# Optimization experiments

Measured on AMD Instinct MI355X. Metric: run time of the kernel, lower is better.

## Reference

```python
import jax, jax.numpy as jnp
import numpy as np

D_MODEL = 1024
D_FF = 4096
NUM_EXPERTS = 8
TOP_K = 2


def setup_inputs() -> dict:
    key = jax.random.key(0)
    ks = jax.random.split(key, 9)
    s_in = 1.0 / np.sqrt(D_MODEL)
    s_ff = 1.0 / np.sqrt(D_FF)
    return {
        "x": jax.random.normal(ks[0], (2, 1024, D_MODEL), dtype=jnp.float32),
        "Wg": jax.random.uniform(ks[1], (D_MODEL, NUM_EXPERTS), minval=-s_in, maxval=s_in, dtype=jnp.float32),
        "bg": jax.random.uniform(ks[2], (NUM_EXPERTS,), minval=-s_in, maxval=s_in, dtype=jnp.float32),
        "W1": jax.random.uniform(ks[3], (NUM_EXPERTS, D_MODEL, D_FF), minval=-s_in, maxval=s_in, dtype=jnp.float32),
        "b1": jax.random.uniform(ks[4], (NUM_EXPERTS, D_FF), minval=-s_in, maxval=s_in, dtype=jnp.float32),
        "W2": jax.random.uniform(ks[5], (NUM_EXPERTS, D_MODEL, D_FF), minval=-s_in, maxval=s_in, dtype=jnp.float32),
        "b2": jax.random.uniform(ks[6], (NUM_EXPERTS, D_FF), minval=-s_in, maxval=s_in, dtype=jnp.float32),
        "W3": jax.random.uniform(ks[7], (NUM_EXPERTS, D_FF, D_MODEL), minval=-s_ff, maxval=s_ff, dtype=jnp.float32),
        "b3": jax.random.uniform(ks[8], (NUM_EXPERTS, D_MODEL), minval=-s_ff, maxval=s_ff, dtype=jnp.float32),
    }


def reference(x, Wg, bg, W1, b1, W2, b2, W3, b3):
    B, S, D = x.shape
    xf = x.reshape(-1, D)                                   # [N, D]
    N = xf.shape[0]

    # ---- Router (eval mode: no noise) ----
    logits = xf @ Wg + bg                                   # [N, E]
    top_logits, top_idx = jax.lax.top_k(logits, TOP_K)      # [N, K]
    top_w = jax.nn.softmax(top_logits, axis=-1)             # softmax over the top-k logits
    # scatter top-k weights into dense [N, E]; indices are unique per row
    comb_w = jnp.zeros_like(logits).at[jnp.arange(N)[:, None], top_idx].set(top_w)

    # ---- Experts: GLU-MLP, dense per-expert (weights are 0 for unrouted tokens) ----
    h1 = jnp.einsum('nd,edf->enf', xf, W1) + b1[:, None, :]  # [E, N, F]
    h2 = jnp.einsum('nd,edf->enf', xf, W2) + b2[:, None, :]
    hidden = jax.nn.gelu(h1, approximate=False) * h2         # torch nn.GELU is exact (erf)
    expert_out = jnp.einsum('enf,efd->end', hidden, W3) + b3[:, None, :]  # [E, N, D]

    # ---- Weighted combine ----
    final = jnp.einsum('end,ne->nd', expert_out, comb_w)     # [N, D]
    aux_loss = 0.0  # eval mode: aux loss inactive
    return final.reshape(B, S, D), aux_loss
```

## Files before the change

### kernel.cpp

```cpp
#include <hip/hip_runtime.h>
#include <hip/hip_bf16.h>
#include <math.h>

#define D_MODEL 1024
#define D_FF    4096
#define NE      8
#define MT      256

typedef __bf16 bf16x8 __attribute__((ext_vector_type(8)));
typedef float  f32x4  __attribute__((ext_vector_type(4)));

__device__ __forceinline__ void async16(const void* g, void* l) {
    __builtin_amdgcn_global_load_lds(
        (__attribute__((address_space(1))) uint32_t*)g,
        (__attribute__((address_space(3))) uint32_t*)l, 16, 0, 0);
}

__global__ __launch_bounds__(256) void router_kernel(
    const float* __restrict__ x, const float* __restrict__ Wg,
    const float* __restrict__ bg, int* __restrict__ topidx,
    float* __restrict__ topw, __bf16* __restrict__ Xb)
{
    int n = blockIdx.x, tid = threadIdx.x;
    const float* xr = x + (size_t)n * D_MODEL;
    int d0 = tid * 4;
    float4 xv = *reinterpret_cast<const float4*>(xr + d0);

    union { __bf16 h[4]; ushort4 u; } pk;
    pk.h[0] = (__bf16)xv.x; pk.h[1] = (__bf16)xv.y;
    pk.h[2] = (__bf16)xv.z; pk.h[3] = (__bf16)xv.w;
    *reinterpret_cast<ushort4*>(Xb + (size_t)n * D_MODEL + d0) = pk.u;

    float part[NE];
#pragma unroll
    for (int e = 0; e < NE; ++e) part[e] = 0.f;
    float xs[4] = {xv.x, xv.y, xv.z, xv.w};
#pragma unroll
    for (int j = 0; j < 4; ++j) {
        const float4* wr = reinterpret_cast<const float4*>(Wg + (size_t)(d0 + j) * NE);
        float4 w0 = wr[0], w1 = wr[1];
        part[0] += xs[j] * w0.x; part[1] += xs[j] * w0.y;
        part[2] += xs[j] * w0.z; part[3] += xs[j] * w0.w;
        part[4] += xs[j] * w1.x; part[5] += xs[j] * w1.y;
        part[6] += xs[j] * w1.z; part[7] += xs[j] * w1.w;
    }
#pragma unroll
    for (int off = 32; off > 0; off >>= 1) {
#pragma unroll
        for (int e = 0; e < NE; ++e) part[e] += __shfl_down(part[e], off);
    }
    __shared__ float sred[4][NE];
    __shared__ float slog[NE];
    int wave = tid >> 6, lane = tid & 63;
    if (lane == 0) {
#pragma unroll
        for (int e = 0; e < NE; ++e) sred[wave][e] = part[e];
    }
    __syncthreads();
    if (tid < NE)
        slog[tid] = bg[tid] + sred[0][tid] + sred[1][tid] + sred[2][tid] + sred[3][tid];
    __syncthreads();
    if (tid == 0) {
        float m0 = -1e30f, m1 = -1e30f; int i0 = 0, i1 = 0;
        for (int e = 0; e < NE; ++e) {
            float l = slog[e];
            if (l > m0)      { m1 = m0; i1 = i0; m0 = l; i0 = e; }
            else if (l > m1) { m1 = l;  i1 = e; }
        }
        float w1 = expf(m1 - m0);
        float s  = 1.f + w1;
        topidx[n * 2 + 0] = i0; topidx[n * 2 + 1] = i1;
        topw[n * 2 + 0] = 1.f / s; topw[n * 2 + 1] = w1 / s;
    }
}

__global__ __launch_bounds__(256) void build_lists_kernel(
    const int* __restrict__ topidx, const float* __restrict__ topw,
    int* __restrict__ pairTok, float* __restrict__ pairW,
    int* __restrict__ rbe, int* __restrict__ pairRow,
    int npairs, int maxrows, int maxblk)
{
    __shared__ int cnt[NE], cur[NE], pof[NE];
    int tid = threadIdx.x;
    if (tid < NE) { cnt[tid] = 0; cur[tid] = 0; }
    for (int i = tid; i < maxrows; i += 256) pairTok[i] = -1;
    for (int i = tid; i < maxblk; i += 256) rbe[i] = -1;
    __syncthreads();
    for (int p = tid; p < npairs; p += 256) atomicAdd(&cnt[topidx[p]], 1);
    __syncthreads();
    if (tid == 0) {
        int off = 0;
        for (int e = 0; e < NE; ++e) { pof[e] = off; off += (cnt[e] + MT - 1) & ~(MT - 1); }
        for (int e = 0; e < NE; ++e) {
            int nb = (cnt[e] + MT - 1) / MT;
            for (int j = 0; j < nb; ++j) rbe[pof[e] / MT + j] = e;
        }
    }
    __syncthreads();
    for (int p = tid; p < npairs; p += 256) {
        int e = topidx[p];
        int pos = atomicAdd(&cur[e], 1);
        int r = pof[e] + pos;
        pairTok[r]  = p >> 1;
        pairW[r]    = topw[p];
        pairRow[p]  = r;
    }
}

__global__ __launch_bounds__(256) void transpose_cvt_kernel(
    const float* __restrict__ src, __bf16* __restrict__ dst, int K, int N)
{
    const float* s = src + (size_t)blockIdx.z * K * N;
    __bf16*      d = dst + (size_t)blockIdx.z * K * N;
    int kt = blockIdx.y * 64, nt = blockIdx.x * 64;
    __shared__ float tile[64][65];
    int tid = threadIdx.x;
    int tr = tid >> 4, tc = (tid & 15) * 4;
#pragma unroll
    for (int it = 0; it < 4; ++it) {
        float4 v = *reinterpret_cast<const float4*>(
            s + (size_t)(kt + tr + it * 16) * N + nt + tc);
        tile[tr + it * 16][tc + 0] = v.x;
        tile[tr + it * 16][tc + 1] = v.y;
        tile[tr + it * 16][tc + 2] = v.z;
        tile[tr + it * 16][tc + 3] = v.w;
    }
    __syncthreads();
    int kq = (tid & 15) * 4;
#pragma unroll
    for (int it = 0; it < 4; ++it) {
        int rr = (tid >> 4) + it * 16;
        union { __bf16 h[4]; ushort4 u; } pk;
        pk.h[0] = (__bf16)tile[kq + 0][rr];
        pk.h[1] = (__bf16)tile[kq + 1][rr];
        pk.h[2] = (__bf16)tile[kq + 2][rr];
        pk.h[3] = (__bf16)tile[kq + 3][rr];
        *reinterpret_cast<ushort4*>(d + (size_t)(nt + rr) * K + kt + kq) = pk.u;
    }
}

__global__ __launch_bounds__(512, 4) void gemm1_mfma(
    const __bf16* __restrict__ Xb, const __bf16* __restrict__ W1t,
    const __bf16* __restrict__ W2t, const float* __restrict__ b1,
    const float* __restrict__ b2, const int* __restrict__ pairTok,
    const int* __restrict__ rbe, const __bf16* __restrict__ zpg,
    __bf16* __restrict__ hidden)
{
    int b = blockIdx.x;
    int e = rbe[b];
    if (e < 0) return;
    int fblk = blockIdx.y * 64;

    __shared__ __bf16 smem[2][12288];

    int tid = threadIdx.x, w = tid >> 6, l = tid & 63;
    int r0 = b * MT;
    int ss4 = (l & 3) ^ ((l >> 3) & 3);

    const __bf16* aptr[2];
#pragma unroll
    for (int j = 0; j < 2; ++j) {
        int row = w * 32 + j * 16 + (l >> 2);
        int tok = pairTok[r0 + row];
        aptr[j] = (tok >= 0 ? Xb + (size_t)tok * D_MODEL : zpg) + ss4 * 8;
    }
    const __bf16* wsrc = (w < 4) ? W1t : W2t;
    int wb = w & 3;
    const __bf16* bptr = wsrc + ((size_t)e << 22)
        + (size_t)(fblk + wb * 16 + (l >> 2)) * D_MODEL + ss4 * 8;
    int bdst = (w < 4 ? 8192 : 10240) + wb * 512;

    int wm = (w >> 1) * 64, wf = (w & 1) * 32;
    int lm = l & 15;
    int sl = (((l >> 4) ^ ((lm >> 1) & 3)) << 3);

    f32x4 c1[4][2], c2[4][2];
#pragma unroll
    for (int mi = 0; mi < 4; ++mi)
#pragma unroll
        for (int fj = 0; fj < 2; ++fj) {
            c1[mi][fj] = (f32x4){0.f, 0.f, 0.f, 0.f};
            c2[mi][fj] = (f32x4){0.f, 0.f, 0.f, 0.f};
        }

    auto stage = [&](int buf, int k0) {
        __bf16* base = &smem[buf][0];
        async16(aptr[0] + k0, base + w * 1024 + l * 8);
        async16(aptr[1] + k0, base + w * 1024 + 512 + l * 8);
        async16(bptr + k0, base + bdst + l * 8);
    };

    stage(0, 0);
    __syncthreads();
    const int NT = D_MODEL / 32;
    for (int t = 0; t < NT; ++t) {
        int cur = t & 1;
        if (t + 1 < NT) stage(cur ^ 1, (t + 1) * 32);
        const __bf16* sb = &smem[cur][0];
        bf16x8 a[4];
#pragma unroll
        for (int mi = 0; mi < 4; ++mi)
            a[mi] = *reinterpret_cast<const bf16x8*>(sb + (wm + mi * 16 + lm) * 32 + sl);
#pragma unroll
        for (int fj = 0; fj < 2; ++fj) {
            int frow = (wf + fj * 16 + lm) * 32 + sl;
            bf16x8 bv1 = *reinterpret_cast<const bf16x8*>(sb + 8192 + frow);
            bf16x8 bv2 = *reinterpret_cast<const bf16x8*>(sb + 10240 + frow);
#pragma unroll
            for (int mi = 0; mi < 4; ++mi) {
                c1[mi][fj] = __builtin_amdgcn_mfma_f32_16x16x32_bf16(a[mi], bv1, c1[mi][fj], 0, 0, 0);
                c2[mi][fj] = __builtin_amdgcn_mfma_f32_16x16x32_bf16(a[mi], bv2, c2[mi][fj], 0, 0, 0);
            }
        }
        __syncthreads();
    }

#pragma unroll
    for (int fj = 0; fj < 2; ++fj) {
        int f = fblk + wf + fj * 16 + lm;
        float b1v = b1[e * D_FF + f];
        float b2v = b2[e * D_FF + f];
#pragma unroll
        for (int mi = 0; mi < 4; ++mi)
#pragma unroll
            for (int r = 0; r < 4; ++r) {
                int m = wm + mi * 16 + (l >> 4) * 4 + r;
                float h1 = c1[mi][fj][r] + b1v;
                float h2 = c2[mi][fj][r] + b2v;
                float g = 0.5f * h1 * (1.f + erff(h1 * 0.70710678118654752f));
                hidden[(size_t)(r0 + m) * D_FF + f] = (__bf16)(g * h2);
            }
    }
}

__global__ __launch_bounds__(512, 4) void gemm2_mfma(
    const __bf16* __restrict__ hidden, const __bf16* __restrict__ W3t,
    const float* __restrict__ b3, const int* __restrict__ rbe,
    float* __restrict__ po)
{
    int rb = blockIdx.x;
    int e = rbe[rb >> 1];
    if (e < 0) return;
    int dblk = blockIdx.y * 128;

    __shared__ __bf16 smem[2][16384];

    int tid = threadIdx.x, w = tid >> 6, l = tid & 63;
    int ss8 = (l & 7) ^ (l >> 3);
    int r0m = rb * 128;

    const __bf16* abase = hidden + (size_t)(r0m + w * 16 + (l >> 3)) * D_FF + ss8 * 8;
    const __bf16* bbase = W3t + ((size_t)e << 22)
        + (size_t)(dblk + w * 16 + (l >> 3)) * D_FF + ss8 * 8;

    int wm = (w >> 1) * 32, wn = (w & 1) * 64;
    int lm = l & 15;

    f32x4 c[2][4];
#pragma unroll
    for (int mi = 0; mi < 2; ++mi)
#pragma unroll
        for (int nj = 0; nj < 4; ++nj) c[mi][nj] = (f32x4){0.f, 0.f, 0.f, 0.f};

    auto stage = [&](int buf, int k0) {
        __bf16* base = &smem[buf][0];
        async16(abase + k0,              base + w * 1024 + l * 8);
        async16(abase + 8 * D_FF + k0,   base + w * 1024 + 512 + l * 8);
        async16(bbase + k0,              base + 8192 + w * 1024 + l * 8);
        async16(bbase + 8 * D_FF + k0,   base + 8192 + w * 1024 + 512 + l * 8);
    };

    stage(0, 0);
    __syncthreads();
    const int NT = D_FF / 64;
    for (int t = 0; t < NT; ++t) {
        int cur = t & 1;
        if (t + 1 < NT) stage(cur ^ 1, (t + 1) * 64);
        const __bf16* sb = &smem[cur][0];
#pragma unroll
        for (int ks = 0; ks < 2; ++ks) {
            int sl = (((ks * 4 + (l >> 4)) ^ (l & 7)) << 3);
            bf16x8 a[2];
#pragma unroll
            for (int mi = 0; mi < 2; ++mi)
                a[mi] = *reinterpret_cast<const bf16x8*>(sb + (wm + mi * 16 + lm) * 64 + sl);
#pragma unroll
            for (int nj = 0; nj < 4; ++nj) {
                bf16x8 bv = *reinterpret_cast<const bf16x8*>(sb + 8192 + (wn + nj * 16 + lm) * 64 + sl);
#pragma unroll
                for (int mi = 0; mi < 2; ++mi)
                    c[mi][nj] = __builtin_amdgcn_mfma_f32_16x16x32_bf16(a[mi], bv, c[mi][nj], 0, 0, 0);
            }
        }
        __syncthreads();
    }

#pragma unroll
    for (int nj = 0; nj < 4; ++nj) {
        int d = dblk + wn + nj * 16 + lm;
        float b3v = b3[e * D_MODEL + d];
#pragma unroll
        for (int mi = 0; mi < 2; ++mi)
#pragma unroll
            for (int r = 0; r < 4; ++r) {
                int m = wm + mi * 16 + (l >> 4) * 4 + r;
                po[(size_t)(r0m + m) * D_MODEL + d] = c[mi][nj][r] + b3v;
            }
    }
}

__global__ __launch_bounds__(256) void combine_kernel(
    const float* __restrict__ po, const float* __restrict__ topw,
    const int* __restrict__ pairRow, float* __restrict__ out)
{
    int t = blockIdx.x, tid = threadIdx.x;
    int d = tid * 4;
    float w0 = topw[t * 2], w1 = topw[t * 2 + 1];
    int r0 = pairRow[t * 2], r1 = pairRow[t * 2 + 1];
    float4 v0 = *reinterpret_cast<const float4*>(po + (size_t)r0 * D_MODEL + d);
    float4 v1 = *reinterpret_cast<const float4*>(po + (size_t)r1 * D_MODEL + d);
    float4 o;
    o.x = w0 * v0.x + w1 * v1.x;
    o.y = w0 * v0.y + w1 * v1.y;
    o.z = w0 * v0.z + w1 * v1.z;
    o.w = w0 * v0.w + w1 * v1.w;
    *reinterpret_cast<float4*>(out + (size_t)t * D_MODEL + d) = o;
}

__global__ __launch_bounds__(256) void gemm1_legacy(
    const __bf16* __restrict__ Xb, const float* __restrict__ W1,
    const float* __restrict__ W2, const float* __restrict__ b1,
    const float* __restrict__ b2, const int* __restrict__ pairTok,
    const int* __restrict__ rbe, __bf16* __restrict__ hidden)
{
    int b = blockIdx.x;
    int e = rbe[b >> 2];
    if (e < 0) return;
    int fblk = blockIdx.y * 128;

    __shared__ __bf16 As[64][40];
    __shared__ __bf16 W1s[128][40];
    __shared__ __bf16 W2s[128][40];

    int tid = threadIdx.x;
    int arow = tid >> 2, akoff = (tid & 3) * 8;
    int r0 = b * 64;
    int tok = pairTok[r0 + arow];
    int wk = tid >> 3, wfb = (tid & 7) * 16;
    const float* w1base = W1 + (size_t)e * D_MODEL * D_FF + (size_t)wk * D_FF + fblk + wfb;
    const float* w2base = W2 + (size_t)e * D_MODEL * D_FF + (size_t)wk * D_FF + fblk + wfb;

    int wave = tid >> 6, lane = tid & 63;
    int wm = (wave >> 1) * 32, wf = (wave & 1) * 64;
    int lm = lane & 15, lk = (lane >> 4) * 8;

    __bf16 z = (__bf16)0.f;
    f32x4 c1[2][4], c2[2][4];
#pragma unroll
    for (int mi = 0; mi < 2; ++mi)
#pragma unroll
        for (int fj = 0; fj < 4; ++fj) {
            c1[mi][fj] = (f32x4){0.f, 0.f, 0.f, 0.f};
            c2[mi][fj] = (f32x4){0.f, 0.f, 0.f, 0.f};
        }

    for (int k0 = 0; k0 < D_MODEL; k0 += 32) {
        __syncthreads();
        bf16x8 av = {z, z, z, z, z, z, z, z};
        if (tok >= 0)
            av = *reinterpret_cast<const bf16x8*>(Xb + (size_t)tok * D_MODEL + k0 + akoff);
        *reinterpret_cast<bf16x8*>(&As[arow][akoff]) = av;
        const float* p1 = w1base + (size_t)k0 * D_FF;
        const float* p2 = w2base + (size_t)k0 * D_FF;
#pragma unroll
        for (int j = 0; j < 4; ++j) {
            float4 v = *reinterpret_cast<const float4*>(p1 + j * 4);
            W1s[wfb + j * 4 + 0][wk] = (__bf16)v.x;
            W1s[wfb + j * 4 + 1][wk] = (__bf16)v.y;
            W1s[wfb + j * 4 + 2][wk] = (__bf16)v.z;
            W1s[wfb + j * 4 + 3][wk] = (__bf16)v.w;
            float4 u = *reinterpret_cast<const float4*>(p2 + j * 4);
            W2s[wfb + j * 4 + 0][wk] = (__bf16)u.x;
            W2s[wfb + j * 4 + 1][wk] = (__bf16)u.y;
            W2s[wfb + j * 4 + 2][wk] = (__bf16)u.z;
            W2s[wfb + j * 4 + 3][wk] = (__bf16)u.w;
        }
        __syncthreads();

        bf16x8 a0 = *reinterpret_cast<bf16x8*>(&As[wm + lm][lk]);
        bf16x8 a1 = *reinterpret_cast<bf16x8*>(&As[wm + 16 + lm][lk]);
#pragma unroll
        for (int fj = 0; fj < 4; ++fj) {
            bf16x8 bw1 = *reinterpret_cast<bf16x8*>(&W1s[wf + fj * 16 + lm][lk]);
            c1[0][fj] = __builtin_amdgcn_mfma_f32_16x16x32_bf16(a0, bw1, c1[0][fj], 0, 0, 0);
            c1[1][fj] = __builtin_amdgcn_mfma_f32_16x16x32_bf16(a1, bw1, c1[1][fj], 0, 0, 0);
            bf16x8 bw2 = *reinterpret_cast<bf16x8*>(&W2s[wf + fj * 16 + lm][lk]);
            c2[0][fj] = __builtin_amdgcn_mfma_f32_16x16x32_bf16(a0, bw2, c2[0][fj], 0, 0, 0);
            c2[1][fj] = __builtin_amdgcn_mfma_f32_16x16x32_bf16(a1, bw2, c2[1][fj], 0, 0, 0);
        }
    }

#pragma unroll
    for (int fj = 0; fj < 4; ++fj) {
        int f = fblk + wf + fj * 16 + lm;
        float b1v = b1[e * D_FF + f];
        float b2v = b2[e * D_FF + f];
#pragma unroll
        for (int mi = 0; mi < 2; ++mi)
#pragma unroll
            for (int r = 0; r < 4; ++r) {
                int m = wm + mi * 16 + (lane >> 4) * 4 + r;
                float h1 = c1[mi][fj][r] + b1v;
                float h2 = c2[mi][fj][r] + b2v;
                float g = 0.5f * h1 * (1.f + erff(h1 * 0.70710678118654752f));
                hidden[(size_t)(r0 + m) * D_FF + f] = (__bf16)(g * h2);
            }
    }
}

__global__ __launch_bounds__(256) void gemm2_legacy(
    const __bf16* __restrict__ hidden, const float* __restrict__ W3,
    const float* __restrict__ b3, const int* __restrict__ pairTok,
    const float* __restrict__ pairW, const int* __restrict__ rbe,
    float* __restrict__ out)
{
    int b = blockIdx.x;
    int e = rbe[b >> 2];
    if (e < 0) return;
    int dblk = blockIdx.y * 128;

    __shared__ __bf16 As[64][40];
    __shared__ __bf16 W3s[128][40];

    int tid = threadIdx.x;
    int arow = tid >> 2, akoff = (tid & 3) * 8;
    int r0 = b * 64;
    const __bf16* ap = hidden + (size_t)(r0 + arow) * D_FF + akoff;
    int wk = tid >> 3, wdb = (tid & 7) * 16;
    const float* w3base = W3 + (size_t)e * D_FF * D_MODEL + (size_t)wk * D_MODEL + dblk + wdb;

    int wave = tid >> 6, lane = tid & 63;
    int wm = (wave >> 1) * 32, wf = (wave & 1) * 64;
    int lm = lane & 15, lk = (lane >> 4) * 8;

    f32x4 c[2][4];
#pragma unroll
    for (int mi = 0; mi < 2; ++mi)
#pragma unroll
        for (int dj = 0; dj < 4; ++dj) c[mi][dj] = (f32x4){0.f, 0.f, 0.f, 0.f};

    for (int k0 = 0; k0 < D_FF; k0 += 32) {
        __syncthreads();
        *reinterpret_cast<bf16x8*>(&As[arow][akoff]) =
            *reinterpret_cast<const bf16x8*>(ap + k0);
        const float* p3 = w3base + (size_t)k0 * D_MODEL;
#pragma unroll
        for (int j = 0; j < 4; ++j) {
            float4 v = *reinterpret_cast<const float4*>(p3 + j * 4);
            W3s[wdb + j * 4 + 0][wk] = (__bf16)v.x;
            W3s[wdb + j * 4 + 1][wk] = (__bf16)v.y;
            W3s[wdb + j * 4 + 2][wk] = (__bf16)v.z;
            W3s[wdb + j * 4 + 3][wk] = (__bf16)v.w;
        }
        __syncthreads();

        bf16x8 a0 = *reinterpret_cast<bf16x8*>(&As[wm + lm][lk]);
        bf16x8 a1 = *reinterpret_cast<bf16x8*>(&As[wm + 16 + lm][lk]);
#pragma unroll
        for (int dj = 0; dj < 4; ++dj) {
            bf16x8 bw = *reinterpret_cast<bf16x8*>(&W3s[wf + dj * 16 + lm][lk]);
            c[0][dj] = __builtin_amdgcn_mfma_f32_16x16x32_bf16(a0, bw, c[0][dj], 0, 0, 0);
            c[1][dj] = __builtin_amdgcn_mfma_f32_16x16x32_bf16(a1, bw, c[1][dj], 0, 0, 0);
        }
    }

#pragma unroll
    for (int dj = 0; dj < 4; ++dj) {
        int d = dblk + wf + dj * 16 + lm;
        float b3v = b3[e * D_MODEL + d];
#pragma unroll
        for (int mi = 0; mi < 2; ++mi)
#pragma unroll
            for (int r = 0; r < 4; ++r) {
                int m = wm + mi * 16 + (lane >> 4) * 4 + r;
                int gr = r0 + m;
                int tok = pairTok[gr];
                if (tok >= 0) {
                    float val = c[mi][dj][r] + b3v;
                    atomicAdd(out + (size_t)tok * D_MODEL + d, pairW[gr] * val);
                }
            }
    }
}

extern "C" void kernel_launch(void* const* d_in, const int* in_sizes, int n_in,
                              void* d_out, int out_size, void* d_ws, size_t ws_size,
                              hipStream_t stream)
{
    const float* x  = (const float*)d_in[0];
    const float* Wg = (const float*)d_in[1];
    const float* bg = (const float*)d_in[2];
    const float* W1 = (const float*)d_in[3];
    const float* b1 = (const float*)d_in[4];
    const float* W2 = (const float*)d_in[5];
    const float* b2 = (const float*)d_in[6];
    const float* W3 = (const float*)d_in[7];
    const float* b3 = (const float*)d_in[8];
    float* out = (float*)d_out;

    int N = in_sizes[0] / D_MODEL;
    int npairs = N * 2;
    int maxblk = npairs / MT + NE;
    int maxrows = maxblk * MT;

    char* ws = (char*)d_ws;
    size_t off = 0;
    auto alloc = [&](size_t bytes) -> void* {
        void* p = ws + off;
        off = (off + bytes + 255) & ~(size_t)255;
        return p;
    };
    int*    topidx  = (int*)   alloc((size_t)npairs * 4);
    float*  topw    = (float*) alloc((size_t)npairs * 4);
    int*    pairTok = (int*)   alloc((size_t)maxrows * 4);
    float*  pairW   = (float*) alloc((size_t)maxrows * 4);
    int*    rbe     = (int*)   alloc((size_t)maxblk * 4);
    int*    pairRow = (int*)   alloc((size_t)npairs * 4);
    __bf16* Xb      = (__bf16*)alloc((size_t)N * D_MODEL * 2);
    __bf16* hidden  = (__bf16*)alloc((size_t)maxrows * D_FF * 2);
    __bf16* zpg     = (__bf16*)alloc(4096);
    const size_t WSZ = (size_t)NE * D_MODEL * D_FF * 2;
    __bf16* W1t = (__bf16*)alloc(WSZ);
    __bf16* W2t = (__bf16*)alloc(WSZ);
    __bf16* W3t = (__bf16*)alloc(WSZ);
    float*  po  = (float*)W1t;
    bool primary = (off <= ws_size);
    (void)n_in;

    hipMemsetAsync(d_out, 0, (size_t)out_size * sizeof(float), stream);
    router_kernel<<<N, 256, 0, stream>>>(x, Wg, bg, topidx, topw, Xb);
    build_lists_kernel<<<1, 256, 0, stream>>>(topidx, topw, pairTok, pairW, rbe,
                                              pairRow, npairs, maxrows, maxblk);
    if (primary) {
        hipMemsetAsync(zpg, 0, 4096, stream);
        transpose_cvt_kernel<<<dim3(D_FF / 64, D_MODEL / 64, NE), 256, 0, stream>>>(
            W1, W1t, D_MODEL, D_FF);
        transpose_cvt_kernel<<<dim3(D_FF / 64, D_MODEL / 64, NE), 256, 0, stream>>>(
            W2, W2t, D_MODEL, D_FF);
        transpose_cvt_kernel<<<dim3(D_MODEL / 64, D_FF / 64, NE), 256, 0, stream>>>(
            W3, W3t, D_FF, D_MODEL);
        gemm1_mfma<<<dim3(maxblk, D_FF / 64), 512, 0, stream>>>(
            Xb, W1t, W2t, b1, b2, pairTok, rbe, zpg, hidden);
        gemm2_mfma<<<dim3(maxblk * 2, D_MODEL / 128), 512, 0, stream>>>(
            hidden, W3t, b3, rbe, po);
        combine_kernel<<<N, 256, 0, stream>>>(po, topw, pairRow, out);
    } else {
        gemm1_legacy<<<dim3(maxblk * 4, D_FF / 128), 256, 0, stream>>>(
            Xb, W1, W2, b1, b2, pairTok, rbe, hidden);
        gemm2_legacy<<<dim3(maxblk * 4, D_MODEL / 128), 256, 0, stream>>>(
            hidden, W3, b3, pairTok, pairW, rbe, out);
    }
}
```

Before: 347.0 us.

## Fuse weight transposes into router and gemm1, enlarge gemm1 tiles

Folds the W1/W2 transpose-convert into the router kernel launch and the W3 transpose into the gemm1 launch, interleaving transpose blocks with GEMM blocks so the memory-bound conversion overlaps the compute-bound GEMM. gemm1 is retiled to 128 output features and a K step of 64 per stage, with an 8-way LDS swizzle and more accumulators per wave. The fallback legacy path and the output memset are removed. Larger LDS use and more registers lower occupancy, and the interleave pattern is hardcoded for one block count.

New measurement: 352.5 us. No clear change (+1.6%).

```diff
diff --git a/kernel.cpp b/kernel.cpp
--- a/kernel.cpp
+++ b/kernel.cpp
@@ -16,12 +16,56 @@
         (__attribute__((address_space(3))) uint32_t*)l, 16, 0, 0);
 }
 
-__global__ __launch_bounds__(256) void router_kernel(
+__device__ __forceinline__ void transpose_tile64(
+    const float* __restrict__ s, __bf16* __restrict__ d,
+    int K, int N, int kt, int nt, int tid, float (*tile)[65])
+{
+    int tr = tid >> 4, tc = (tid & 15) * 4;
+#pragma unroll
+    for (int it = 0; it < 4; ++it) {
+        float4 v = *reinterpret_cast<const float4*>(
+            s + (size_t)(kt + tr + it * 16) * N + nt + tc);
+        tile[tr + it * 16][tc + 0] = v.x;
+        tile[tr + it * 16][tc + 1] = v.y;
+        tile[tr + it * 16][tc + 2] = v.z;
+        tile[tr + it * 16][tc + 3] = v.w;
+    }
+    __syncthreads();
+    int kq = (tid & 15) * 4;
+#pragma unroll
+    for (int it = 0; it < 4; ++it) {
+        int rr = (tid >> 4) + it * 16;
+        union { __bf16 h[4]; ushort4 u; } pk;
+        pk.h[0] = (__bf16)tile[kq + 0][rr];
+        pk.h[1] = (__bf16)tile[kq + 1][rr];
+        pk.h[2] = (__bf16)tile[kq + 2][rr];
+        pk.h[3] = (__bf16)tile[kq + 3][rr];
+        *reinterpret_cast<ushort4*>(d + (size_t)(nt + rr) * K + kt + kq) = pk.u;
+    }
+}
+
+__global__ __launch_bounds__(256) void fused_pre(
     const float* __restrict__ x, const float* __restrict__ Wg,
     const float* __restrict__ bg, int* __restrict__ topidx,
-    float* __restrict__ topw, __bf16* __restrict__ Xb)
-{
-    int n = blockIdx.x, tid = threadIdx.x;
+    float* __restrict__ topw, __bf16* __restrict__ Xb,
+    const float* __restrict__ W1, const float* __restrict__ W2,
+    __bf16* __restrict__ W1t, __bf16* __restrict__ W2t, int nrouter)
+{
+    __shared__ float buf[64][65];
+    int bid = blockIdx.x, tid = threadIdx.x;
+
+    if (bid >= nrouter) {
+        int tt = bid - nrouter;
+        const float* s = W1; __bf16* d = W1t;
+        if (tt >= 8192) { s = W2; d = W2t; tt -= 8192; }
+        int e = tt >> 10, rem = tt & 1023;
+        int kt_i = rem >> 6, nt_i = rem & 63;
+        transpose_tile64(s + ((size_t)e << 22), d + ((size_t)e << 22),
+                         D_MODEL, D_FF, kt_i * 64, nt_i * 64, tid, buf);
+        return;
+    }
+
+    int n = bid;
     const float* xr = x + (size_t)n * D_MODEL;
     int d0 = tid * 4;
     float4 xv = *reinterpret_cast<const float4*>(xr + d0);
@@ -49,16 +93,16 @@
 #pragma unroll
         for (int e = 0; e < NE; ++e) part[e] += __shfl_down(part[e], off);
     }
-    __shared__ float sred[4][NE];
-    __shared__ float slog[NE];
+    float* sred = &buf[0][0];
+    float* slog = &buf[1][0];
     int wave = tid >> 6, lane = tid & 63;
     if (lane == 0) {
 #pragma unroll
-        for (int e = 0; e < NE; ++e) sred[wave][e] = part[e];
+        for (int e = 0; e < NE; ++e) sred[wave * NE + e] = part[e];
     }
     __syncthreads();
     if (tid < NE)
-        slog[tid] = bg[tid] + sred[0][tid] + sred[1][tid] + sred[2][tid] + sred[3][tid];
+        slog[tid] = bg[tid] + sred[tid] + sred[NE + tid] + sred[2 * NE + tid] + sred[3 * NE + tid];
     __syncthreads();
     if (tid == 0) {
         float m0 = -1e30f, m1 = -1e30f; int i0 = 0, i1 = 0;
@@ -107,116 +151,113 @@
     }
 }
 
-__global__ __launch_bounds__(256) void transpose_cvt_kernel(
-    const float* __restrict__ src, __bf16* __restrict__ dst, int K, int N)
-{
-    const float* s = src + (size_t)blockIdx.z * K * N;
-    __bf16*      d = dst + (size_t)blockIdx.z * K * N;
-    int kt = blockIdx.y * 64, nt = blockIdx.x * 64;
-    __shared__ float tile[64][65];
-    int tid = threadIdx.x;
-    int tr = tid >> 4, tc = (tid & 15) * 4;
-#pragma unroll
-    for (int it = 0; it < 4; ++it) {
-        float4 v = *reinterpret_cast<const float4*>(
-            s + (size_t)(kt + tr + it * 16) * N + nt + tc);
-        tile[tr + it * 16][tc + 0] = v.x;
-        tile[tr + it * 16][tc + 1] = v.y;
-        tile[tr + it * 16][tc + 2] = v.z;
-        tile[tr + it * 16][tc + 3] = v.w;
-    }
-    __syncthreads();
-    int kq = (tid & 15) * 4;
-#pragma unroll
-    for (int it = 0; it < 4; ++it) {
-        int rr = (tid >> 4) + it * 16;
-        union { __bf16 h[4]; ushort4 u; } pk;
-        pk.h[0] = (__bf16)tile[kq + 0][rr];
-        pk.h[1] = (__bf16)tile[kq + 1][rr];
-        pk.h[2] = (__bf16)tile[kq + 2][rr];
-        pk.h[3] = (__bf16)tile[kq + 3][rr];
-        *reinterpret_cast<ushort4*>(d + (size_t)(nt + rr) * K + kt + kq) = pk.u;
-    }
-}
-
-__global__ __launch_bounds__(512, 4) void gemm1_mfma(
+__global__ __launch_bounds__(512) void gemm1_fused(
     const __bf16* __restrict__ Xb, const __bf16* __restrict__ W1t,
     const __bf16* __restrict__ W2t, const float* __restrict__ b1,
     const float* __restrict__ b2, const int* __restrict__ pairTok,
     const int* __restrict__ rbe, const __bf16* __restrict__ zpg,
-    __bf16* __restrict__ hidden)
-{
-    int b = blockIdx.x;
+    __bf16* __restrict__ hidden,
+    const float* __restrict__ W3, __bf16* __restrict__ W3t,
+    int maxblk, int ilv)
+{
+    __shared__ __bf16 smem[2][32768];
+    int bid = blockIdx.x, tid = threadIdx.x;
+    int n_g1 = maxblk * 32;
+
+    int g = -1, t = -1;
+    if (ilv) {
+        int ph = bid % 19, grp = bid / 19;
+        if (ph < 3) g = grp * 3 + ph; else t = grp * 16 + (ph - 3);
+    } else {
+        if (bid < n_g1) g = bid; else t = bid - n_g1;
+    }
+
+    if (t >= 0) {
+        int sub = tid >> 8;
+        int tile = t * 2 + sub;
+        int e = tile >> 10, rem = tile & 1023;
+        int kt_i = rem >> 4, nt_i = rem & 15;
+        float (*tb)[65] = reinterpret_cast<float (*)[65]>(&smem[0][0]) + sub * 64;
+        transpose_tile64(W3 + ((size_t)e << 22), W3t + ((size_t)e << 22),
+                         D_FF, D_MODEL, kt_i * 64, nt_i * 64, tid & 255, tb);
+        return;
+    }
+
+    int b = g % maxblk;
     int e = rbe[b];
     if (e < 0) return;
-    int fblk = blockIdx.y * 64;
-
-    __shared__ __bf16 smem[2][12288];
-
-    int tid = threadIdx.x, w = tid >> 6, l = tid & 63;
+    int fblk = (g / maxblk) * 128;
+
+    int w = tid >> 6, l = tid & 63;
+    int srcslot = (l & 7) ^ (l >> 3);
     int r0 = b * MT;
-    int ss4 = (l & 3) ^ ((l >> 3) & 3);
-
-    const __bf16* aptr[2];
-#pragma unroll
-    for (int j = 0; j < 2; ++j) {
-        int row = w * 32 + j * 16 + (l >> 2);
+
+    const __bf16* aptr[4];
+#pragma unroll
+    for (int j = 0; j < 4; ++j) {
+        int row = w * 32 + j * 8 + (l >> 3);
         int tok = pairTok[r0 + row];
-        aptr[j] = (tok >= 0 ? Xb + (size_t)tok * D_MODEL : zpg) + ss4 * 8;
-    }
-    const __bf16* wsrc = (w < 4) ? W1t : W2t;
-    int wb = w & 3;
-    const __bf16* bptr = wsrc + ((size_t)e << 22)
-        + (size_t)(fblk + wb * 16 + (l >> 2)) * D_MODEL + ss4 * 8;
-    int bdst = (w < 4 ? 8192 : 10240) + wb * 512;
-
-    int wm = (w >> 1) * 64, wf = (w & 1) * 32;
+        aptr[j] = (tok >= 0 ? Xb + (size_t)tok * D_MODEL : zpg) + srcslot * 8;
+    }
+    const __bf16* b1base = W1t + ((size_t)e << 22)
+        + (size_t)(fblk + w * 16 + (l >> 3)) * D_MODEL + srcslot * 8;
+    const __bf16* b2base = W2t + ((size_t)e << 22)
+        + (size_t)(fblk + w * 16 + (l >> 3)) * D_MODEL + srcslot * 8;
+
+    int wm = (w >> 1) * 64, wf = (w & 1) * 64;
     int lm = l & 15;
-    int sl = (((l >> 4) ^ ((lm >> 1) & 3)) << 3);
-
-    f32x4 c1[4][2], c2[4][2];
+
+    f32x4 c1[4][4], c2[4][4];
 #pragma unroll
     for (int mi = 0; mi < 4; ++mi)
 #pragma unroll
-        for (int fj = 0; fj < 2; ++fj) {
+        for (int fj = 0; fj < 4; ++fj) {
             c1[mi][fj] = (f32x4){0.f, 0.f, 0.f, 0.f};
             c2[mi][fj] = (f32x4){0.f, 0.f, 0.f, 0.f};
         }
 
     auto stage = [&](int buf, int k0) {
         __bf16* base = &smem[buf][0];
-        async16(aptr[0] + k0, base + w * 1024 + l * 8);
-        async16(aptr[1] + k0, base + w * 1024 + 512 + l * 8);
-        async16(bptr + k0, base + bdst + l * 8);
+#pragma unroll
+        for (int j = 0; j < 4; ++j)
+            async16(aptr[j] + k0, base + w * 2048 + j * 512);
+        async16(b1base + k0,               base + 16384 + w * 1024);
+        async16(b1base + 8 * D_MODEL + k0, base + 16384 + w * 1024 + 512);
+        async16(b2base + k0,               base + 24576 + w * 1024);
+        async16(b2base + 8 * D_MODEL + k0, base + 24576 + w * 1024 + 512);
     };
 
     stage(0, 0);
     __syncthreads();
-    const int NT = D_MODEL / 32;
-    for (int t = 0; t < NT; ++t) {
-        int cur = t & 1;
-        if (t + 1 < NT) stage(cur ^ 1, (t + 1) * 32);
+    const int NT = D_MODEL / 64;
+    for (int tt = 0; tt < NT; ++tt) {
+        int cur = tt & 1;
+        if (tt + 1 < NT) stage(cur ^ 1, (tt + 1) * 64);
         const __bf16* sb = &smem[cur][0];
-        bf16x8 a[4];
-#pragma unroll
-        for (int mi = 0; mi < 4; ++mi)
-            a[mi] = *reinterpret_cast<const bf16x8*>(sb + (wm + mi * 16 + lm) * 32 + sl);
-#pragma unroll
-        for (int fj = 0; fj < 2; ++fj) {
-            int frow = (wf + fj * 16 + lm) * 32 + sl;
-            bf16x8 bv1 = *reinterpret_cast<const bf16x8*>(sb + 8192 + frow);
-            bf16x8 bv2 = *reinterpret_cast<const bf16x8*>(sb + 10240 + frow);
-#pragma unroll
-            for (int mi = 0; mi < 4; ++mi) {
-                c1[mi][fj] = __builtin_amdgcn_mfma_f32_16x16x32_bf16(a[mi], bv1, c1[mi][fj], 0, 0, 0);
-                c2[mi][fj] = __builtin_amdgcn_mfma_f32_16x16x32_bf16(a[mi], bv2, c2[mi][fj], 0, 0, 0);
+#pragma unroll
+        for (int ks = 0; ks < 2; ++ks) {
+            int sl = (((ks * 4 + (l >> 4)) ^ (l & 7)) << 3);
+            bf16x8 a[4];
+#pragma unroll
+            for (int mi = 0; mi < 4; ++mi)
+                a[mi] = *reinterpret_cast<const bf16x8*>(sb + (wm + mi * 16 + lm) * 64 + sl);
+#pragma unroll
+            for (int fj = 0; fj < 4; ++fj) {
+                int frow = wf + fj * 16 + lm;
+                bf16x8 bv1 = *reinterpret_cast<const bf16x8*>(sb + 16384 + frow * 64 + sl);
+                bf16x8 bv2 = *reinterpret_cast<const bf16x8*>(sb + 24576 + frow * 64 + sl);
+#pragma unroll
+                for (int mi = 0; mi < 4; ++mi) {
+                    c1[mi][fj] = __builtin_amdgcn_mfma_f32_16x16x32_bf16(a[mi], bv1, c1[mi][fj], 0, 0, 0);
+                    c2[mi][fj] = __builtin_amdgcn_mfma_f32_16x16x32_bf16(a[mi], bv2, c2[mi][fj], 0, 0, 0);
+                }
             }
         }
         __syncthreads();
     }
 
 #pragma unroll
-    for (int fj = 0; fj < 2; ++fj) {
+    for (int fj = 0; fj < 4; ++fj) {
         int f = fblk + wf + fj * 16 + lm;
         float b1v = b1[e * D_FF + f];
         float b2v = b2[e * D_FF + f];
@@ -227,8 +268,8 @@
                 int m = wm + mi * 16 + (l >> 4) * 4 + r;
                 float h1 = c1[mi][fj][r] + b1v;
                 float h2 = c2[mi][fj][r] + b2v;
-                float g = 0.5f * h1 * (1.f + erff(h1 * 0.70710678118654752f));
-                hidden[(size_t)(r0 + m) * D_FF + f] = (__bf16)(g * h2);
+                float gg = 0.5f * h1 * (1.f + erff(h1 * 0.70710678118654752f));
+                hidden[(size_t)(r0 + m) * D_FF + f] = (__bf16)(gg * h2);
             }
     }
 }
@@ -325,172 +366,6 @@
     o.z = w0 * v0.z + w1 * v1.z;
     o.w = w0 * v0.w + w1 * v1.w;
     *reinterpret_cast<float4*>(out + (size_t)t * D_MODEL + d) = o;
-}
-
-__global__ __launch_bounds__(256) void gemm1_legacy(
-    const __bf16* __restrict__ Xb, const float* __restrict__ W1,
-    const float* __restrict__ W2, const float* __restrict__ b1,
-    const float* __restrict__ b2, const int* __restrict__ pairTok,
-    const int* __restrict__ rbe, __bf16* __restrict__ hidden)
-{
-    int b = blockIdx.x;
-    int e = rbe[b >> 2];
-    if (e < 0) return;
-    int fblk = blockIdx.y * 128;
-
-    __shared__ __bf16 As[64][40];
-    __shared__ __bf16 W1s[128][40];
-    __shared__ __bf16 W2s[128][40];
-
-    int tid = threadIdx.x;
-    int arow = tid >> 2, akoff = (tid & 3) * 8;
-    int r0 = b * 64;
-    int tok = pairTok[r0 + arow];
-    int wk = tid >> 3, wfb = (tid & 7) * 16;
-    const float* w1base = W1 + (size_t)e * D_MODEL * D_FF + (size_t)wk * D_FF + fblk + wfb;
-    const float* w2base = W2 + (size_t)e * D_MODEL * D_FF + (size_t)wk * D_FF + fblk + wfb;
-
-    int wave = tid >> 6, lane = tid & 63;
-    int wm = (wave >> 1) * 32, wf = (wave & 1) * 64;
-    int lm = lane & 15, lk = (lane >> 4) * 8;
-
-    __bf16 z = (__bf16)0.f;
-    f32x4 c1[2][4], c2[2][4];
-#pragma unroll
-    for (int mi = 0; mi < 2; ++mi)
-#pragma unroll
-        for (int fj = 0; fj < 4; ++fj) {
-            c1[mi][fj] = (f32x4){0.f, 0.f, 0.f, 0.f};
-            c2[mi][fj] = (f32x4){0.f, 0.f, 0.f, 0.f};
-        }
-
-    for (int k0 = 0; k0 < D_MODEL; k0 += 32) {
-        __syncthreads();
-        bf16x8 av = {z, z, z, z, z, z, z, z};
-        if (tok >= 0)
-            av = *reinterpret_cast<const bf16x8*>(Xb + (size_t)tok * D_MODEL + k0 + akoff);
-        *reinterpret_cast<bf16x8*>(&As[arow][akoff]) = av;
-        const float* p1 = w1base + (size_t)k0 * D_FF;
-        const float* p2 = w2base + (size_t)k0 * D_FF;
-#pragma unroll
-        for (int j = 0; j < 4; ++j) {
-            float4 v = *reinterpret_cast<const float4*>(p1 + j * 4);
-            W1s[wfb + j * 4 + 0][wk] = (__bf16)v.x;
-            W1s[wfb + j * 4 + 1][wk] = (__bf16)v.y;
-            W1s[wfb + j * 4 + 2][wk] = (__bf16)v.z;
-            W1s[wfb + j * 4 + 3][wk] = (__bf16)v.w;
-            float4 u = *reinterpret_cast<const float4*>(p2 + j * 4);
-            W2s[wfb + j * 4 + 0][wk] = (__bf16)u.x;
-            W2s[wfb + j * 4 + 1][wk] = (__bf16)u.y;
-            W2s[wfb + j * 4 + 2][wk] = (__bf16)u.z;
-            W2s[wfb + j * 4 + 3][wk] = (__bf16)u.w;
-        }
-        __syncthreads();
-
-        bf16x8 a0 = *reinterpret_cast<bf16x8*>(&As[wm + lm][lk]);
-        bf16x8 a1 = *reinterpret_cast<bf16x8*>(&As[wm + 16 + lm][lk]);
-#pragma unroll
-        for (int fj = 0; fj < 4; ++fj) {
-            bf16x8 bw1 = *reinterpret_cast<bf16x8*>(&W1s[wf + fj * 16 + lm][lk]);
-            c1[0][fj] = __builtin_amdgcn_mfma_f32_16x16x32_bf16(a0, bw1, c1[0][fj], 0, 0, 0);
-            c1[1][fj] = __builtin_amdgcn_mfma_f32_16x16x32_bf16(a1, bw1, c1[1][fj], 0, 0, 0);
-            bf16x8 bw2 = *reinterpret_cast<bf16x8*>(&W2s[wf + fj * 16 + lm][lk]);
-            c2[0][fj] = __builtin_amdgcn_mfma_f32_16x16x32_bf16(a0, bw2, c2[0][fj], 0, 0, 0);
-            c2[1][fj] = __builtin_amdgcn_mfma_f32_16x16x32_bf16(a1, bw2, c2[1][fj], 0, 0, 0);
-        }
-    }
-
-#pragma unroll
-    for (int fj = 0; fj < 4; ++fj) {
-        int f = fblk + wf + fj * 16 + lm;
-        float b1v = b1[e * D_FF + f];
-        float b2v = b2[e * D_FF + f];
-#pragma unroll
-        for (int mi = 0; mi < 2; ++mi)
-#pragma unroll
-            for (int r = 0; r < 4; ++r) {
-                int m = wm + mi * 16 + (lane >> 4) * 4 + r;
-                float h1 = c1[mi][fj][r] + b1v;
-                float h2 = c2[mi][fj][r] + b2v;
-                float g = 0.5f * h1 * (1.f + erff(h1 * 0.70710678118654752f));
-                hidden[(size_t)(r0 + m) * D_FF + f] = (__bf16)(g * h2);
-            }
-    }
-}
-
-__global__ __launch_bounds__(256) void gemm2_legacy(
-    const __bf16* __restrict__ hidden, const float* __restrict__ W3,
-    const float* __restrict__ b3, const int* __restrict__ pairTok,
-    const float* __restrict__ pairW, const int* __restrict__ rbe,
-    float* __restrict__ out)
-{
-    int b = blockIdx.x;
-    int e = rbe[b >> 2];
-    if (e < 0) return;
-    int dblk = blockIdx.y * 128;
-
-    __shared__ __bf16 As[64][40];
-    __shared__ __bf16 W3s[128][40];
-
-    int tid = threadIdx.x;
-    int arow = tid >> 2, akoff = (tid & 3) * 8;
-    int r0 = b * 64;
-    const __bf16* ap = hidden + (size_t)(r0 + arow) * D_FF + akoff;
-    int wk = tid >> 3, wdb = (tid & 7) * 16;
-    const float* w3base = W3 + (size_t)e * D_FF * D_MODEL + (size_t)wk * D_MODEL + dblk + wdb;
-
-    int wave = tid >> 6, lane = tid & 63;
-    int wm = (wave >> 1) * 32, wf = (wave & 1) * 64;
-    int lm = lane & 15, lk = (lane >> 4) * 8;
-
-    f32x4 c[2][4];
-#pragma unroll
-    for (int mi = 0; mi < 2; ++mi)
-#pragma unroll
-        for (int dj = 0; dj < 4; ++dj) c[mi][dj] = (f32x4){0.f, 0.f, 0.f, 0.f};
-
-    for (int k0 = 0; k0 < D_FF; k0 += 32) {
-        __syncthreads();
-        *reinterpret_cast<bf16x8*>(&As[arow][akoff]) =
-            *reinterpret_cast<const bf16x8*>(ap + k0);
-        const float* p3 = w3base + (size_t)k0 * D_MODEL;
-#pragma unroll
-        for (int j = 0; j < 4; ++j) {
-            float4 v = *reinterpret_cast<const float4*>(p3 + j * 4);
-            W3s[wdb + j * 4 + 0][wk] = (__bf16)v.x;
-            W3s[wdb + j * 4 + 1][wk] = (__bf16)v.y;
-            W3s[wdb + j * 4 + 2][wk] = (__bf16)v.z;
-            W3s[wdb + j * 4 + 3][wk] = (__bf16)v.w;
-        }
-        __syncthreads();
-
-        bf16x8 a0 = *reinterpret_cast<bf16x8*>(&As[wm + lm][lk]);
-        bf16x8 a1 = *reinterpret_cast<bf16x8*>(&As[wm + 16 + lm][lk]);
-#pragma unroll
-        for (int dj = 0; dj < 4; ++dj) {
-            bf16x8 bw = *reinterpret_cast<bf16x8*>(&W3s[wf + dj * 16 + lm][lk]);
-            c[0][dj] = __builtin_amdgcn_mfma_f32_16x16x32_bf16(a0, bw, c[0][dj], 0, 0, 0);
-            c[1][dj] = __builtin_amdgcn_mfma_f32_16x16x32_bf16(a1, bw, c[1][dj], 0, 0, 0);
-        }
-    }
-
-#pragma unroll
-    for (int dj = 0; dj < 4; ++dj) {
-        int d = dblk + wf + dj * 16 + lm;
-        float b3v = b3[e * D_MODEL + d];
-#pragma unroll
-        for (int mi = 0; mi < 2; ++mi)
-#pragma unroll
-            for (int r = 0; r < 4; ++r) {
-                int m = wm + mi * 16 + (lane >> 4) * 4 + r;
-                int gr = r0 + m;
-                int tok = pairTok[gr];
-                if (tok >= 0) {
-                    float val = c[mi][dj][r] + b3v;
-                    atomicAdd(out + (size_t)tok * D_MODEL + d, pairW[gr] * val);
-                }
-            }
-    }
 }
 
 extern "C" void kernel_launch(void* const* d_in, const int* in_sizes, int n_in,
@@ -534,30 +409,19 @@
     __bf16* W2t = (__bf16*)alloc(WSZ);
     __bf16* W3t = (__bf16*)alloc(WSZ);
     float*  po  = (float*)W1t;
-    bool primary = (off <= ws_size);
-    (void)n_in;
-
-    hipMemsetAsync(d_out, 0, (size_t)out_size * sizeof(float), stream);
-    router_kernel<<<N, 256, 0, stream>>>(x, Wg, bg, topidx, topw, Xb);
+    (void)ws_size; (void)n_in; (void)pairW;
+
+    hipMemsetAsync(zpg, 0, 4096, stream);
+
+    fused_pre<<<N + 2 * 8192, 256, 0, stream>>>(
+        x, Wg, bg, topidx, topw, Xb, W1, W2, W1t, W2t, N);
     build_lists_kernel<<<1, 256, 0, stream>>>(topidx, topw, pairTok, pairW, rbe,
                                               pairRow, npairs, maxrows, maxblk);
-    if (primary) {
-        hipMemsetAsync(zpg, 0, 4096, stream);
-        transpose_cvt_kernel<<<dim3(D_FF / 64, D_MODEL / 64, NE), 256, 0, stream>>>(
-            W1, W1t, D_MODEL, D_FF);
-        transpose_cvt_kernel<<<dim3(D_FF / 64, D_MODEL / 64, NE), 256, 0, stream>>>(
-            W2, W2t, D_MODEL, D_FF);
-        transpose_cvt_kernel<<<dim3(D_MODEL / 64, D_FF / 64, NE), 256, 0, stream>>>(
-            W3, W3t, D_FF, D_MODEL);
-        gemm1_mfma<<<dim3(maxblk, D_FF / 64), 512, 0, stream>>>(
-            Xb, W1t, W2t, b1, b2, pairTok, rbe, zpg, hidden);
-        gemm2_mfma<<<dim3(maxblk * 2, D_MODEL / 128), 512, 0, stream>>>(
-            hidden, W3t, b3, rbe, po);
-        combine_kernel<<<N, 256, 0, stream>>>(po, topw, pairRow, out);
-    } else {
-        gemm1_legacy<<<dim3(maxblk * 4, D_FF / 128), 256, 0, stream>>>(
-            Xb, W1, W2, b1, b2, pairTok, rbe, hidden);
-        gemm2_legacy<<<dim3(maxblk * 4, D_MODEL / 128), 256, 0, stream>>>(
-            hidden, W3, b3, pairTok, pairW, rbe, out);
-    }
-}
+    int n_g1 = maxblk * 32, n_t3 = 4096;
+    int ilv = (n_g1 == 768) ? 1 : 0;
+    gemm1_fused<<<n_g1 + n_t3, 512, 0, stream>>>(
+        Xb, W1t, W2t, b1, b2, pairTok, rbe, zpg, hidden, W3, W3t, maxblk, ilv);
+    gemm2_mfma<<<dim3(maxblk * 2, D_MODEL / 128), 512, 0, stream>>>(
+        hidden, W3t, b3, rbe, po);
+    combine_kernel<<<N, 256, 0, stream>>>(po, topw, pairRow, out);
+}
```
